# Kernel tuning notes

Measured on AMD Instinct MI355X. Metric: run time of the kernel, lower is better.

## Reference

```python
import jax, jax.numpy as jnp
import numpy as np

C_IN = 256
GROUP = C_IN // 4  # module hard-codes group = C_in/4 -> 4 channels per group
EPS = 1e-5

@jax.custom_vjp
def binarize(x):
    # 1-bit quantization: sign forward, hardtanh straight-through backward
    return jnp.sign(x)

def _bin_fwd(x):
    return jnp.sign(x), x

def _bin_bwd(x, g):
    return (g * (jnp.abs(x) <= 1.0).astype(g.dtype),)

binarize.defvjp(_bin_fwd, _bin_bwd)

def channel_shuffle(x, g):
    # [N,C,H,W] -> [N,g,C/g,H,W] -> [N,C/g,g,H,W] -> [N,C,H,W]
    N, C, H, W = x.shape
    return x.reshape(N, g, C // g, H, W).transpose(0, 2, 1, 3, 4).reshape(N, C, H, W)


def setup_inputs() -> dict:
    key = jax.random.key(0)
    ks = jax.random.split(key, 6)
    x = jax.random.normal(ks[0], (32, C_IN, 56, 56), jnp.float32)
    # grouped conv weight: [C_out, C_in/group, kH, kW] = [256, 4, 3, 3]
    weight = jax.random.normal(ks[1], (C_IN, C_IN // GROUP, 3, 3), jnp.float32) * 0.1
    gamma = 1.0 + 0.1 * jax.random.normal(ks[2], (C_IN,), jnp.float32)
    beta = 0.1 * jax.random.normal(ks[3], (C_IN,), jnp.float32)
    running_mean = 0.1 * jax.random.normal(ks[4], (C_IN,), jnp.float32)
    running_var = jax.random.uniform(ks[5], (C_IN,), jnp.float32, 0.5, 1.5)
    return dict(x=x, weight=weight, gamma=gamma, beta=beta,
                running_mean=running_mean, running_var=running_var)


def reference(x, weight, gamma, beta, running_mean, running_var):
    # BatchNorm2d (inference-mode, affine=True)
    inv = gamma * jax.lax.rsqrt(running_var + EPS)
    xb = x * inv[None, :, None, None] + (beta - running_mean * inv)[None, :, None, None]
    # Conv2d_1w1a: binarize activations and weights, grouped 3x3 conv, no bias
    a = binarize(xb)
    w = binarize(weight)
    out = jax.lax.conv_general_dilated(
        a, w,
        window_strides=(1, 1),
        padding=((1, 1), (1, 1)),
        dimension_numbers=('NCHW', 'OIHW', 'NCHW'),
        feature_group_count=GROUP,
    )
    out = channel_shuffle(out, GROUP)
    # stride == 1 -> shortcut is identity
    return out + x
```

## Files before the change

### kernel.cpp

```cpp
#include <hip/hip_runtime.h>
#include <stdint.h>

#define H 56
#define W 56
#define HW (H * W)
#define CIN 256
#define IMG (CIN * HW)
#define EPS 1e-5f

#define ROWW 8
#define TR2 30
#define TSZ (TR2 * ROWW)
#define ATASKS 406
#define BTASKS 392

__device__ __forceinline__ float mul_rn(float a, float b) {
    float d; asm("v_mul_f32 %0, %1, %2" : "=v"(d) : "v"(a), "v"(b)); return d;
}
__device__ __forceinline__ float add_rn(float a, float b) {
    float d; asm("v_add_f32 %0, %1, %2" : "=v"(d) : "v"(a), "v"(b)); return d;
}
__device__ __forceinline__ float sub_rn(float a, float b) {
    float d; asm("v_sub_f32 %0, %1, %2" : "=v"(d) : "v"(a), "v"(b)); return d;
}
__device__ __forceinline__ float mul_rn_sv(float s, float v) {
    float d; asm("v_mul_f32 %0, %1, %2" : "=v"(d) : "s"(s), "v"(v)); return d;
}
__device__ __forceinline__ float add_rn_sv(float s, float v) {
    float d; asm("v_add_f32 %0, %1, %2" : "=v"(d) : "s"(s), "v"(v)); return d;
}
__device__ __forceinline__ float rfl_f(float x) {
    return __int_as_float(__builtin_amdgcn_readfirstlane(__float_as_int(x)));
}


__global__ __launch_bounds__(256)
void binconv_kernel(const float* __restrict__ X,
                    const float* __restrict__ Wt,
                    const float* __restrict__ gamma,
                    const float* __restrict__ beta,
                    const float* __restrict__ mean,
                    const float* __restrict__ var,
                    float* __restrict__ out) {
    __shared__ uint32_t s_tile[TSZ];
    __shared__ uint32_t z_tile[TSZ];
    __shared__ uint32_t ws_l[4][3];
    __shared__ uint32_t wz_l[4][3];

    const int bx   = blockIdx.x;
    const int half = bx & 1;
    const int g    = (bx >> 1) & 63;
    const int n    = bx >> 7;
    const int tid  = threadIdx.x;

    for (int i = tid; i < 2 * TSZ; i += 256) {
        if (i < TSZ) s_tile[i] = 0u;
        else         z_tile[i - TSZ] = 0u;
    }

    if (tid < 4) {
        const float* wc = Wt + (size_t)(g * 4 + tid) * 36;
        for (int r = 0; r < 3; ++r) {
            uint32_t s = 0, z = 0;
            for (int ci = 0; ci < 4; ++ci)
                for (int kw = 0; kw < 3; ++kw) {
                    float v = wc[ci * 9 + r * 3 + kw];
                    int b = kw * 4 + ci;
                    s |= (v > 0.f  ? 1u : 0u) << b;
                    z |= (v != 0.f ? 1u : 0u) << b;
                }
            ws_l[tid][r] = s; wz_l[tid][r] = z;
        }
    }

    float inv[4], bias[4];
#pragma unroll
    for (int ci = 0; ci < 4; ++ci) {
        int c = g * 4 + ci;
        float s  = sqrtf(var[c] + EPS);
        float r  = 1.0f / s;
        float iv = mul_rn(gamma[c], r);
        inv[ci]  = rfl_f(iv);
        bias[ci] = rfl_f(sub_rn(beta[c], mul_rn(mean[c], iv)));
    }

    const float* Xn = X   + (size_t)n * IMG;
    float*       On = out + (size_t)n * IMG;

    __syncthreads();

    const int rowbase = half * 27;
    const int rtoff   = 1 - half;
    for (int task = tid; task < ATASKS; task += 256) {
        int ar = task / 14;
        int cg = task - ar * 14;
        int off = (rowbase + ar) * W + cg * 4;
        uint32_t s16 = 0, z16 = 0;
#pragma unroll
        for (int ci = 0; ci < 4; ++ci) {
            const float4 v = *reinterpret_cast<const float4*>(
                Xn + (size_t)(g * 4 + ci) * HW + off);
            float t0 = add_rn_sv(bias[ci], mul_rn_sv(inv[ci], v.x));
            float t1 = add_rn_sv(bias[ci], mul_rn_sv(inv[ci], v.y));
            float t2 = add_rn_sv(bias[ci], mul_rn_sv(inv[ci], v.z));
            float t3 = add_rn_sv(bias[ci], mul_rn_sv(inv[ci], v.w));
            s16 |= ((t0 > 0.f ? 1u : 0u) << ci)        | ((t1 > 0.f ? 1u : 0u) << (4 + ci))
                 | ((t2 > 0.f ? 1u : 0u) << (8 + ci))  | ((t3 > 0.f ? 1u : 0u) << (12 + ci));
            z16 |= ((t0 != 0.f ? 1u : 0u) << ci)       | ((t1 != 0.f ? 1u : 0u) << (4 + ci))
                 | ((t2 != 0.f ? 1u : 0u) << (8 + ci)) | ((t3 != 0.f ? 1u : 0u) << (12 + ci));
        }
        int rt = ar + rtoff;
        reinterpret_cast<uint16_t*>(&s_tile[rt * ROWW])[cg] = (uint16_t)s16;
        reinterpret_cast<uint16_t*>(&z_tile[rt * ROWW])[cg] = (uint16_t)z16;
    }

    uint32_t wsj[4][3], wzj[4][3];
    bool full = true;
#pragma unroll
    for (int j = 0; j < 4; ++j)
#pragma unroll
        for (int r = 0; r < 3; ++r) {
            wsj[j][r] = __builtin_amdgcn_readfirstlane(ws_l[j][r]);
            wzj[j][r] = __builtin_amdgcn_readfirstlane(wz_l[j][r]);
            full = full && (wzj[j][r] == 0xFFFu);
        }

    __syncthreads();

    for (int task = tid; task < BTASKS; task += 256) {
        int hl = task / 14;
        int cg = task - hl * 14;
        int w0 = cg * 4;
        size_t pbase = (size_t)(half * 28 + hl) * W + w0;

        uint64_t vs[3], vz[3];
        int off;
        if (w0 == 0) {
            off = 0;
#pragma unroll
            for (int r = 0; r < 3; ++r) {
                int base = (hl + r) * ROWW;
                vs[r] = (((uint64_t)s_tile[base] | ((uint64_t)s_tile[base + 1] << 32)) << 4);
                vz[r] = (((uint64_t)z_tile[base] | ((uint64_t)z_tile[base + 1] << 32)) << 4);
            }
        } else {
            int st = 4 * w0 - 4;
            int i0 = st >> 5;
            off = st & 31;
#pragma unroll
            for (int r = 0; r < 3; ++r) {
                int base = (hl + r) * ROWW + i0;
                vs[r] = ((uint64_t)s_tile[base] | ((uint64_t)s_tile[base + 1] << 32));
                vz[r] = ((uint64_t)z_tile[base] | ((uint64_t)z_tile[base + 1] << 32));
            }
        }

        float4 sc[4];
#pragma unroll
        for (int j = 0; j < 4; ++j)
            sc[j] = *reinterpret_cast<const float4*>(Xn + (size_t)(j * 64 + g) * HW + pbase);

        int res[4][4];
        if (full) {
#pragma unroll
            for (int k = 0; k < 4; ++k) {
                int sh = off + 4 * k;
                uint32_t s0 = (uint32_t)(vs[0] >> sh) & 0xFFFu;
                uint32_t s1 = (uint32_t)(vs[1] >> sh) & 0xFFFu;
                uint32_t s2 = (uint32_t)(vs[2] >> sh) & 0xFFFu;
                uint32_t z0 = (uint32_t)(vz[0] >> sh) & 0xFFFu;
                uint32_t z1 = (uint32_t)(vz[1] >> sh) & 0xFFFu;
                uint32_t z2 = (uint32_t)(vz[2] >> sh) & 0xFFFu;
                int vb = __popc(z0) + __popc(z1) + __popc(z2);
#pragma unroll
                for (int j = 0; j < 4; ++j) {
                    int pc = __popc((s0 ^ wsj[j][0]) & z0)
                           + __popc((s1 ^ wsj[j][1]) & z1)
                           + __popc((s2 ^ wsj[j][2]) & z2);
                    res[j][k] = vb - 2 * pc;
                }
            }
        } else {
#pragma unroll
            for (int k = 0; k < 4; ++k) {
                int sh = off + 4 * k;
                uint32_t s0 = (uint32_t)(vs[0] >> sh) & 0xFFFu;
                uint32_t s1 = (uint32_t)(vs[1] >> sh) & 0xFFFu;
                uint32_t s2 = (uint32_t)(vs[2] >> sh) & 0xFFFu;
                uint32_t z0 = (uint32_t)(vz[0] >> sh) & 0xFFFu;
                uint32_t z1 = (uint32_t)(vz[1] >> sh) & 0xFFFu;
                uint32_t z2 = (uint32_t)(vz[2] >> sh) & 0xFFFu;
#pragma unroll
                for (int j = 0; j < 4; ++j) {
                    uint32_t m0 = z0 & wzj[j][0];
                    uint32_t m1 = z1 & wzj[j][1];
                    uint32_t m2 = z2 & wzj[j][2];
                    int vb = __popc(m0) + __popc(m1) + __popc(m2);
                    int pc = __popc((s0 ^ wsj[j][0]) & m0)
                           + __popc((s1 ^ wsj[j][1]) & m1)
                           + __popc((s2 ^ wsj[j][2]) & m2);
                    res[j][k] = vb - 2 * pc;
                }
            }
        }

#pragma unroll
        for (int j = 0; j < 4; ++j) {
            size_t cofs = (size_t)(j * 64 + g) * HW + pbase;
            float4 o;
            o.x = add_rn((float)res[j][0], sc[j].x);
            o.y = add_rn((float)res[j][1], sc[j].y);
            o.z = add_rn((float)res[j][2], sc[j].z);
            o.w = add_rn((float)res[j][3], sc[j].w);
            *reinterpret_cast<float4*>(On + cofs) = o;
        }
    }
}

extern "C" void kernel_launch(void* const* d_in, const int* in_sizes, int n_in,
                              void* d_out, int out_size, void* d_ws, size_t ws_size,
                              hipStream_t stream) {
    const float* X     = (const float*)d_in[0];
    const float* Wt    = (const float*)d_in[1];
    const float* gamma = (const float*)d_in[2];
    const float* beta  = (const float*)d_in[3];
    const float* mean  = (const float*)d_in[4];
    const float* var   = (const float*)d_in[5];
    float* out = (float*)d_out;

    int N = in_sizes[0] / IMG;

    binconv_kernel<<<N * 64 * 2, 256, 0, stream>>>(X, Wt, gamma, beta, mean, var, out);
}
```

Baseline: 201.5 us.

## Use 384-thread blocks, prefetch first input tile early, remap block order across batch

Raises the block size from 256 to 384 threads so most A and B tasks finish in one pass, and issues the first input-tile loads before zeroing shared memory and building the weight masks, so load latency overlaps that setup. BN parameters are read as float4 vectors, weight binarization is split across 12 threads, and block indices are remapped so 8 consecutive blocks cover 8 different images. The cost is more registers held across the prologue, plus the new launch bound and block mapping, which change occupancy and cache locality. The remapped index assumes N is a multiple of 8.

```diff
diff --git a/kernel.cpp b/kernel.cpp
--- a/kernel.cpp
+++ b/kernel.cpp
@@ -13,6 +13,7 @@
 #define TSZ (TR2 * ROWW)
 #define ATASKS 406
 #define BTASKS 392
+#define NT 384
 
 __device__ __forceinline__ float mul_rn(float a, float b) {
     float d; asm("v_mul_f32 %0, %1, %2" : "=v"(d) : "v"(a), "v"(b)); return d;
@@ -34,7 +35,7 @@
 }
 
 
-__global__ __launch_bounds__(256)
+__global__ __launch_bounds__(NT, 8)
 void binconv_kernel(const float* __restrict__ X,
                     const float* __restrict__ Wt,
                     const float* __restrict__ gamma,
@@ -48,58 +49,94 @@
     __shared__ uint32_t wz_l[4][3];
 
     const int bx   = blockIdx.x;
-    const int half = bx & 1;
-    const int g    = (bx >> 1) & 63;
-    const int n    = bx >> 7;
+    const int n    = ((bx >> 10) << 3) | (bx & 7);
+    const int rem  = (bx >> 3) & 127;
+    const int g    = rem >> 1;
+    const int half = rem & 1;
     const int tid  = threadIdx.x;
 
-    for (int i = tid; i < 2 * TSZ; i += 256) {
+    const int rowbase = half * 27;
+    const int rtoff   = 1 - half;
+
+    const float* Xn = X   + (size_t)n * IMG;
+    float*       On = out + (size_t)n * IMG;
+
+    const int ar0 = tid / 14;
+    const int cg0 = tid - ar0 * 14;
+    const float* p0 = Xn + (size_t)(g * 4) * HW + (rowbase + ar0) * W + cg0 * 4;
+    float4 q0[4];
+#pragma unroll
+    for (int ci = 0; ci < 4; ++ci)
+        q0[ci] = *reinterpret_cast<const float4*>(p0 + (size_t)ci * HW);
+
+    const float4 vv = *reinterpret_cast<const float4*>(var   + g * 4);
+    const float4 vg = *reinterpret_cast<const float4*>(gamma + g * 4);
+    const float4 vb = *reinterpret_cast<const float4*>(beta  + g * 4);
+    const float4 vm = *reinterpret_cast<const float4*>(mean  + g * 4);
+
+    for (int i = tid; i < 2 * TSZ; i += NT) {
         if (i < TSZ) s_tile[i] = 0u;
         else         z_tile[i - TSZ] = 0u;
     }
 
-    if (tid < 4) {
-        const float* wc = Wt + (size_t)(g * 4 + tid) * 36;
-        for (int r = 0; r < 3; ++r) {
-            uint32_t s = 0, z = 0;
-            for (int ci = 0; ci < 4; ++ci)
-                for (int kw = 0; kw < 3; ++kw) {
-                    float v = wc[ci * 9 + r * 3 + kw];
-                    int b = kw * 4 + ci;
-                    s |= (v > 0.f  ? 1u : 0u) << b;
-                    z |= (v != 0.f ? 1u : 0u) << b;
-                }
-            ws_l[tid][r] = s; wz_l[tid][r] = z;
-        }
+    if (tid < 12) {
+        int j = tid / 3, r = tid - j * 3;
+        const float* wc = Wt + (size_t)(g * 4 + j) * 36 + r * 3;
+        uint32_t s = 0, z = 0;
+        for (int ci = 0; ci < 4; ++ci)
+            for (int kw = 0; kw < 3; ++kw) {
+                float v = wc[ci * 9 + kw];
+                int b = kw * 4 + ci;
+                s |= (v > 0.f  ? 1u : 0u) << b;
+                z |= (v != 0.f ? 1u : 0u) << b;
+            }
+        ws_l[j][r] = s; wz_l[j][r] = z;
     }
 
     float inv[4], bias[4];
+    {
+        const float va[4] = {vv.x, vv.y, vv.z, vv.w};
+        const float ga[4] = {vg.x, vg.y, vg.z, vg.w};
+        const float ba[4] = {vb.x, vb.y, vb.z, vb.w};
+        const float ma[4] = {vm.x, vm.y, vm.z, vm.w};
+#pragma unroll
+        for (int ci = 0; ci < 4; ++ci) {
+            float s  = sqrtf(va[ci] + EPS);
+            float r  = 1.0f / s;
+            float iv = mul_rn(ga[ci], r);
+            inv[ci]  = rfl_f(iv);
+            bias[ci] = rfl_f(sub_rn(ba[ci], mul_rn(ma[ci], iv)));
+        }
+    }
+
+    uint32_t s16_0 = 0, z16_0 = 0;
 #pragma unroll
     for (int ci = 0; ci < 4; ++ci) {
-        int c = g * 4 + ci;
-        float s  = sqrtf(var[c] + EPS);
-        float r  = 1.0f / s;
-        float iv = mul_rn(gamma[c], r);
-        inv[ci]  = rfl_f(iv);
-        bias[ci] = rfl_f(sub_rn(beta[c], mul_rn(mean[c], iv)));
-    }
-
-    const float* Xn = X   + (size_t)n * IMG;
-    float*       On = out + (size_t)n * IMG;
+        float t0 = add_rn_sv(bias[ci], mul_rn_sv(inv[ci], q0[ci].x));
+        float t1 = add_rn_sv(bias[ci], mul_rn_sv(inv[ci], q0[ci].y));
+        float t2 = add_rn_sv(bias[ci], mul_rn_sv(inv[ci], q0[ci].z));
+        float t3 = add_rn_sv(bias[ci], mul_rn_sv(inv[ci], q0[ci].w));
+        s16_0 |= ((t0 > 0.f ? 1u : 0u) << ci)        | ((t1 > 0.f ? 1u : 0u) << (4 + ci))
+               | ((t2 > 0.f ? 1u : 0u) << (8 + ci))  | ((t3 > 0.f ? 1u : 0u) << (12 + ci));
+        z16_0 |= ((t0 != 0.f ? 1u : 0u) << ci)       | ((t1 != 0.f ? 1u : 0u) << (4 + ci))
+               | ((t2 != 0.f ? 1u : 0u) << (8 + ci)) | ((t3 != 0.f ? 1u : 0u) << (12 + ci));
+    }
 
     __syncthreads();
 
-    const int rowbase = half * 27;
-    const int rtoff   = 1 - half;
-    for (int task = tid; task < ATASKS; task += 256) {
-        int ar = task / 14;
-        int cg = task - ar * 14;
-        int off = (rowbase + ar) * W + cg * 4;
+    {
+        int rt = ar0 + rtoff;
+        reinterpret_cast<uint16_t*>(&s_tile[rt * ROWW])[cg0] = (uint16_t)s16_0;
+        reinterpret_cast<uint16_t*>(&z_tile[rt * ROWW])[cg0] = (uint16_t)z16_0;
+    }
+    for (int t = tid + NT; t < ATASKS; t += NT) {
+        int ar = t / 14;
+        int cg = t - ar * 14;
+        const float* p = Xn + (size_t)(g * 4) * HW + (rowbase + ar) * W + cg * 4;
         uint32_t s16 = 0, z16 = 0;
 #pragma unroll
         for (int ci = 0; ci < 4; ++ci) {
-            const float4 v = *reinterpret_cast<const float4*>(
-                Xn + (size_t)(g * 4 + ci) * HW + off);
+            const float4 v = *reinterpret_cast<const float4*>(p + (size_t)ci * HW);
             float t0 = add_rn_sv(bias[ci], mul_rn_sv(inv[ci], v.x));
             float t1 = add_rn_sv(bias[ci], mul_rn_sv(inv[ci], v.y));
             float t2 = add_rn_sv(bias[ci], mul_rn_sv(inv[ci], v.z));
@@ -127,7 +164,7 @@
 
     __syncthreads();
 
-    for (int task = tid; task < BTASKS; task += 256) {
+    for (int task = tid; task < BTASKS; task += NT) {
         int hl = task / 14;
         int cg = task - hl * 14;
         int w0 = cg * 4;
@@ -230,5 +267,5 @@
 
     int N = in_sizes[0] / IMG;
 
-    binconv_kernel<<<N * 64 * 2, 256, 0, stream>>>(X, Wt, gamma, beta, mean, var, out);
-}
+    binconv_kernel<<<N * 64 * 2, NT, 0, stream>>>(X, Wt, gamma, beta, mean, var, out);
+}
```

New measurement: 200.6 us. No clear change (-0.4%).
